# Kernel tuning notes

Hardware: AMD Instinct MI355X
Metric: run time of the kernel (lower is better)

The kernel has to match this reference:

```python
import jax, jax.numpy as jnp
import numpy as np

NUM_HEADS = 6
WIN = 16
NW = 16   # number of windows sharing one mask (b_ % NW == 0)


def setup_inputs() -> dict:
    key = jax.random.key(0)
    ks = jax.random.split(key, 6)
    b_, n, dim = 256, WIN * WIN, 192
    qkv = jax.random.normal(ks[0], (b_, n, 3 * dim), dtype=jnp.float32)
    rpi = jax.random.randint(ks[1], (n, n), 0, (2 * WIN - 1) * (2 * WIN - 1))
    # additive attention mask per window-group (Swin uses 0 / -100; randn is fine for math)
    mask = jax.random.normal(ks[2], (NW, n, n), dtype=jnp.float32)
    rpb_table = 0.02 * jax.random.normal(ks[3], ((2 * WIN - 1) * (2 * WIN - 1), NUM_HEADS), dtype=jnp.float32)
    proj_w = jax.random.normal(ks[4], (dim, dim), dtype=jnp.float32) * (1.0 / np.sqrt(dim))
    proj_b = jax.random.normal(ks[5], (dim,), dtype=jnp.float32) * 0.01
    return {"qkv": qkv, "rpi": rpi, "mask": mask, "rpb_table": rpb_table,
            "proj_w": proj_w, "proj_b": proj_b}


def reference(qkv, rpi, mask, rpb_table, proj_w, proj_b):
    b_, n, c3 = qkv.shape
    c = c3 // 3
    h = NUM_HEADS
    hd = c // h
    scale = float(hd) ** -0.5
    # (b_, n, 3, h, hd) -> (3, b_, h, n, hd)
    qkv = qkv.reshape(b_, n, 3, h, hd).transpose(2, 0, 3, 1, 4)
    q, k, v = qkv[0] * scale, qkv[1], qkv[2]
    attn = jnp.einsum('bhqd,bhkd->bhqk', q, k)  # [b_, h, n, n]
    # gathered relative position bias: [n, n, h] -> [h, n, n]
    bias = rpb_table[rpi].transpose(2, 0, 1)
    attn = attn + bias[None]
    # add per-window-group mask: [b_//nw, nw, h, n, n]
    nw = mask.shape[0]
    attn = attn.reshape(b_ // nw, nw, h, n, n) + mask[None, :, None]
    attn = attn.reshape(b_, h, n, n)
    attn = jax.nn.softmax(attn, axis=-1)
    x = jnp.einsum('bhqk,bhkd->bhqd', attn, v)  # [b_, h, n, hd]
    x = x.transpose(0, 2, 1, 3).reshape(b_, n, c)
    # nn.Linear: x @ W^T + b
    return x @ proj_w.T + proj_b
```

## Files before the change

### kernel.cpp

```cpp
#include <hip/hip_runtime.h>
#include <hip/hip_bf16.h>

typedef _Float16 f16;
typedef _Float16 f16x2 __attribute__((ext_vector_type(2)));
typedef _Float16 f16x4 __attribute__((ext_vector_type(4)));
typedef _Float16 f16x8 __attribute__((ext_vector_type(8)));
typedef __fp16 h16x2 __attribute__((ext_vector_type(2)));
typedef float f32x4 __attribute__((ext_vector_type(4)));

#define NHEADS 6
#define NTOK 256
#define NWINS 256
#define DIM 192
#define HD 32
#define C3 576
#define LOG2E 1.4426950408889634f
#define SCALE (0.17677669529663687f * LOG2E)

__device__ inline f16x2 pkrtz(float a, float b) {
  h16x2 r = __builtin_amdgcn_cvt_pkrtz(a, b);
  return __builtin_bit_cast(f16x2, r);
}

__global__ __launch_bounds__(256) void prep_cb_kernel(const int* __restrict__ rpi,
                                                      const float* __restrict__ mask,
                                                      const float* __restrict__ rpb,
                                                      f16* __restrict__ cb) {
  int idx = blockIdx.x * 256 + threadIdx.x;
  int k = idx & 255;
  int q = (idx >> 8) & 255;
  int t = idx >> 16;
  int h = t % 6;
  int mg = t / 6;
  float v = (rpb[rpi[(q << 8) | k] * 6 + h] + mask[(mg << 16) | (q << 8) | k]) * LOG2E;
  cb[idx] = (f16)v;
}

__global__ __launch_bounds__(256) void prep_w_kernel(const float* __restrict__ w,
                                                     f16* __restrict__ w16) {
  int i = blockIdx.x * 256 + threadIdx.x;
  if (i < DIM * DIM) w16[i] = (f16)w[i];
}

__device__ inline f16x8 q_to_f16(float4 a, float4 b) {
  f16x2 p0 = pkrtz(a.x * SCALE, a.y * SCALE);
  f16x2 p1 = pkrtz(a.z * SCALE, a.w * SCALE);
  f16x2 p2 = pkrtz(b.x * SCALE, b.y * SCALE);
  f16x2 p3 = pkrtz(b.z * SCALE, b.w * SCALE);
  f16x4 lo = __builtin_shufflevector(p0, p1, 0, 1, 2, 3);
  f16x4 hi = __builtin_shufflevector(p2, p3, 0, 1, 2, 3);
  return __builtin_shufflevector(lo, hi, 0, 1, 2, 3, 4, 5, 6, 7);
}

__global__ __launch_bounds__(256, 3) void attn_kernel(const float* __restrict__ qkv,
                                                      const f16* __restrict__ cb,
                                                      f16* __restrict__ x16) {
  const int idx = blockIdx.x;
  const int b = idx & 255;
  const int h = idx >> 8;
  const int tid = threadIdx.x;
  const int lane = tid & 63;
  const int wave = tid >> 6;
  const int g = lane >> 4;
  const int r16 = lane & 15;

  __shared__ f16 Klin[16 * 64 * 8];
  __shared__ f16 VT[32][264];

  const int qbase = wave * 64;
  const size_t cb_base = ((size_t)((b & 15) * 6 + h)) << 16;
  const f16* cbp = cb + cb_base + ((size_t)(qbase + r16) << 8) + g * 4;

  const int srow = tid >> 3;
  const int part = tid & 7;
  const float* kbase = qkv + (size_t)(b * NTOK + srow) * C3 + DIM + h * HD + part * 4;
  float4 ka[4], va[4], kb[4], vb[4];
#pragma unroll
  for (int rg = 0; rg < 4; ++rg) {
    const float* kp = kbase + (size_t)(rg * 32) * C3;
    ka[rg] = *(const float4*)kp;
    va[rg] = *(const float4*)(kp + DIM);
  }
#pragma unroll
  for (int rg = 0; rg < 4; ++rg) {
    const float* kp = kbase + (size_t)(rg * 32 + 128) * C3;
    kb[rg] = *(const float4*)kp;
    vb[rg] = *(const float4*)(kp + DIM);
  }

  f16x4 cv[16];
#pragma unroll
  for (int i = 0; i < 16; ++i) cv[i] = *((const f16x4*)(cbp + i * 16));

  const float* qp = qkv + (size_t)(b * NTOK + qbase + r16) * C3 + h * HD + g * 8;
  float4 qn0 = ((const float4*)qp)[0];
  float4 qn1 = ((const float4*)qp)[1];

  const int gg = part >> 1;
  const int half = part & 1;
  const int d0 = part * 4;
#pragma unroll
  for (int rg = 0; rg < 4; ++rg) {
    const int row = rg * 32 + srow;
    const int slot = ((row >> 4) * 64) + gg * 16 + ((row & 15) ^ (gg << 2));
    f16x2 k01 = pkrtz(ka[rg].x, ka[rg].y);
    f16x2 k23 = pkrtz(ka[rg].z, ka[rg].w);
    *((f16x4*)&Klin[slot * 8 + half * 4]) = __builtin_shufflevector(k01, k23, 0, 1, 2, 3);
    VT[d0 + 0][row ^ (((d0 + 0) & 7) << 2)] = (f16)va[rg].x;
    VT[d0 + 1][row ^ (((d0 + 1) & 7) << 2)] = (f16)va[rg].y;
    VT[d0 + 2][row ^ (((d0 + 2) & 7) << 2)] = (f16)va[rg].z;
    VT[d0 + 3][row ^ (((d0 + 3) & 7) << 2)] = (f16)va[rg].w;
  }
#pragma unroll
  for (int rg = 0; rg < 4; ++rg) {
    const int row = rg * 32 + srow + 128;
    const int slot = ((row >> 4) * 64) + gg * 16 + ((row & 15) ^ (gg << 2));
    f16x2 k01 = pkrtz(kb[rg].x, kb[rg].y);
    f16x2 k23 = pkrtz(kb[rg].z, kb[rg].w);
    *((f16x4*)&Klin[slot * 8 + half * 4]) = __builtin_shufflevector(k01, k23, 0, 1, 2, 3);
    VT[d0 + 0][row ^ (((d0 + 0) & 7) << 2)] = (f16)vb[rg].x;
    VT[d0 + 1][row ^ (((d0 + 1) & 7) << 2)] = (f16)vb[rg].y;
    VT[d0 + 2][row ^ (((d0 + 2) & 7) << 2)] = (f16)vb[rg].z;
    VT[d0 + 3][row ^ (((d0 + 3) & 7) << 2)] = (f16)vb[rg].w;
  }

  f16x8 qf = q_to_f16(qn0, qn1);

  __syncthreads();

  const int krd = (lane & 48) + ((lane & 15) ^ ((lane >> 2) & 12));

#pragma unroll
  for (int c = 0; c < 4; ++c) {
    f32x4 acc[16];
#pragma unroll
    for (int kt = 0; kt < 16; ++kt) {
      acc[kt][0] = 0.f; acc[kt][1] = 0.f; acc[kt][2] = 0.f; acc[kt][3] = 0.f;
    }
#pragma unroll
    for (int kt = 0; kt < 16; ++kt) {
      f16x8 af = *((const f16x8*)&Klin[(kt * 64 + krd) * 8]);
      acc[kt] = __builtin_amdgcn_mfma_f32_16x16x32_f16(af, qf, acc[kt], 0, 0, 0);
    }

    float m0 = -1e30f, m1 = -1e30f, m2 = -1e30f, m3 = -1e30f;
#pragma unroll
    for (int kt = 0; kt < 16; ++kt) {
      acc[kt][0] += (float)cv[kt][0];
      acc[kt][1] += (float)cv[kt][1];
      acc[kt][2] += (float)cv[kt][2];
      acc[kt][3] += (float)cv[kt][3];
      m0 = fmaxf(m0, acc[kt][0]);
      m1 = fmaxf(m1, acc[kt][1]);
      m2 = fmaxf(m2, acc[kt][2]);
      m3 = fmaxf(m3, acc[kt][3]);
    }

    if (c < 3) {
      const f16* cbn = cbp + (c + 1) * 4096;
#pragma unroll
      for (int i = 0; i < 16; ++i) cv[i] = *((const f16x4*)(cbn + i * 16));
      const float* qpn = qp + (size_t)((c + 1) * 16) * C3;
      qn0 = ((const float4*)qpn)[0];
      qn1 = ((const float4*)qpn)[1];
    }

    float m = fmaxf(fmaxf(m0, m1), fmaxf(m2, m3));
    m = fmaxf(m, __shfl_xor(m, 16));
    m = fmaxf(m, __shfl_xor(m, 32));

    float s0 = 0.f, s1 = 0.f, s2 = 0.f, s3 = 0.f;
#pragma unroll
    for (int kt = 0; kt < 16; ++kt) {
      float p0 = __builtin_amdgcn_exp2f(acc[kt][0] - m);
      float p1 = __builtin_amdgcn_exp2f(acc[kt][1] - m);
      float p2 = __builtin_amdgcn_exp2f(acc[kt][2] - m);
      float p3 = __builtin_amdgcn_exp2f(acc[kt][3] - m);
      acc[kt][0] = p0; acc[kt][1] = p1; acc[kt][2] = p2; acc[kt][3] = p3;
      s0 += p0; s1 += p1; s2 += p2; s3 += p3;
    }
    float s = (s0 + s1) + (s2 + s3);
    s += __shfl_xor(s, 16);
    s += __shfl_xor(s, 32);
    const float rinv = 1.0f / s;

    f32x4 xacc[2];
#pragma unroll
    for (int dt = 0; dt < 2; ++dt) {
      xacc[dt][0] = 0.f; xacc[dt][1] = 0.f; xacc[dt][2] = 0.f; xacc[dt][3] = 0.f;
    }
#pragma unroll
    for (int kt = 0; kt < 16; ++kt) {
      f16x2 p01 = pkrtz(acc[kt][0], acc[kt][1]);
      f16x2 p23 = pkrtz(acc[kt][2], acc[kt][3]);
      f16x4 pf = __builtin_shufflevector(p01, p23, 0, 1, 2, 3);
#pragma unroll
      for (int dt = 0; dt < 2; ++dt) {
        const int vrow = dt * 16 + r16;
        const int col = (kt * 16 + g * 4) ^ ((r16 & 7) << 2);
        f16x4 vf = *((const f16x4*)&VT[vrow][col]);
        xacc[dt] = __builtin_amdgcn_mfma_f32_16x16x16f16(vf, pf, xacc[dt], 0, 0, 0);
      }
    }

    f16* xp = x16 + (size_t)(b * NTOK + qbase + c * 16 + r16) * DIM + h * HD;
#pragma unroll
    for (int dt = 0; dt < 2; ++dt) {
      f16x2 o01 = pkrtz(xacc[dt][0] * rinv, xacc[dt][1] * rinv);
      f16x2 o23 = pkrtz(xacc[dt][2] * rinv, xacc[dt][3] * rinv);
      *((f16x4*)(xp + dt * 16 + g * 4)) = __builtin_shufflevector(o01, o23, 0, 1, 2, 3);
    }

    if (c < 3) qf = q_to_f16(qn0, qn1);
  }
}

__global__ __launch_bounds__(256) void proj_kernel(const f16* __restrict__ x16,
                                                   const f16* __restrict__ w16,
                                                   const float* __restrict__ pb,
                                                   float* __restrict__ out) {
  const int lane = threadIdx.x & 63;
  const int wave = threadIdx.x >> 6;
  const int g = lane >> 4;
  const int r16 = lane & 15;
  const int m0 = blockIdx.x * 64 + wave * 16;

  f32x4 acc[12];
#pragma unroll
  for (int jt = 0; jt < 12; ++jt) {
    acc[jt][0] = 0.f; acc[jt][1] = 0.f; acc[jt][2] = 0.f; acc[jt][3] = 0.f;
  }
#pragma unroll
  for (int cc = 0; cc < 6; ++cc) {
    f16x8 af = *((const f16x8*)(x16 + (size_t)(m0 + r16) * DIM + cc * 32 + g * 8));
#pragma unroll
    for (int jt = 0; jt < 12; ++jt) {
      f16x8 bf = *((const f16x8*)(w16 + (size_t)(jt * 16 + r16) * DIM + cc * 32 + g * 8));
      acc[jt] = __builtin_amdgcn_mfma_f32_16x16x32_f16(af, bf, acc[jt], 0, 0, 0);
    }
  }
#pragma unroll
  for (int jt = 0; jt < 12; ++jt) {
    int j = jt * 16 + r16;
    float bias = pb[j];
#pragma unroll
    for (int r = 0; r < 4; ++r) {
      out[(size_t)(m0 + g * 4 + r) * DIM + j] = acc[jt][r] + bias;
    }
  }
}

extern "C" void kernel_launch(void* const* d_in, const int* in_sizes, int n_in,
                              void* d_out, int out_size, void* d_ws, size_t ws_size,
                              hipStream_t stream) {
  const float* qkv  = (const float*)d_in[0];
  const int*   rpi  = (const int*)d_in[1];
  const float* mask = (const float*)d_in[2];
  const float* rpb  = (const float*)d_in[3];
  const float* pw   = (const float*)d_in[4];
  const float* pbv  = (const float*)d_in[5];
  float* out = (float*)d_out;

  char* ws = (char*)d_ws;
  f16* cb  = (f16*)ws;
  f16* x16 = (f16*)(ws + 12582912);
  f16* w16 = (f16*)(ws + 12582912 + 25165824);

  prep_cb_kernel<<<24576, 256, 0, stream>>>(rpi, mask, rpb, cb);
  prep_w_kernel<<<144, 256, 0, stream>>>(pw, w16);
  attn_kernel<<<1536, 256, 0, stream>>>(qkv, cb, x16);
  proj_kernel<<<1024, 256, 0, stream>>>(x16, w16, pbv, out);
}
```

Before: 122.3 us.

## Split key loop into two online-softmax halves to raise attention occupancy

Each 16-query chunk now handles its 256 keys as two halves of 128, using an online-softmax rescale (scA) to merge the two partial results. This halves the live accumulator and bias registers, allowing launch bounds to rise from 3 to 4 blocks per SIMD. The exchange is extra exp/rescale arithmetic, an additional cross-lane max reduction per chunk, and serialisation between the halves.

```diff
diff --git a/kernel.cpp b/kernel.cpp
--- a/kernel.cpp
+++ b/kernel.cpp
@@ -52,7 +52,7 @@
   return __builtin_shufflevector(lo, hi, 0, 1, 2, 3, 4, 5, 6, 7);
 }
 
-__global__ __launch_bounds__(256, 3) void attn_kernel(const float* __restrict__ qkv,
+__global__ __launch_bounds__(256, 4) void attn_kernel(const float* __restrict__ qkv,
                                                       const f16* __restrict__ cb,
                                                       f16* __restrict__ x16) {
   const int idx = blockIdx.x;
@@ -88,9 +88,9 @@
     vb[rg] = *(const float4*)(kp + DIM);
   }
 
-  f16x4 cv[16];
-#pragma unroll
-  for (int i = 0; i < 16; ++i) cv[i] = *((const f16x4*)(cbp + i * 16));
+  f16x4 cvA[8], cvB[8];
+#pragma unroll
+  for (int i = 0; i < 8; ++i) cvA[i] = *((const f16x4*)(cbp + i * 16));
 
   const float* qp = qkv + (size_t)(b * NTOK + qbase + r16) * C3 + h * HD + g * 8;
   float4 qn0 = ((const float4*)qp)[0];
@@ -132,46 +132,105 @@
 
 #pragma unroll
   for (int c = 0; c < 4; ++c) {
-    f32x4 acc[16];
-#pragma unroll
-    for (int kt = 0; kt < 16; ++kt) {
+    f32x4 acc[8];
+#pragma unroll
+    for (int kt = 0; kt < 8; ++kt) {
       acc[kt][0] = 0.f; acc[kt][1] = 0.f; acc[kt][2] = 0.f; acc[kt][3] = 0.f;
     }
 #pragma unroll
-    for (int kt = 0; kt < 16; ++kt) {
+    for (int kt = 0; kt < 8; ++kt) {
       f16x8 af = *((const f16x8*)&Klin[(kt * 64 + krd) * 8]);
       acc[kt] = __builtin_amdgcn_mfma_f32_16x16x32_f16(af, qf, acc[kt], 0, 0, 0);
     }
 
+    const f16* cbc = cbp + c * 4096;
+#pragma unroll
+    for (int i = 0; i < 8; ++i) cvB[i] = *((const f16x4*)(cbc + (8 + i) * 16));
+
     float m0 = -1e30f, m1 = -1e30f, m2 = -1e30f, m3 = -1e30f;
 #pragma unroll
-    for (int kt = 0; kt < 16; ++kt) {
-      acc[kt][0] += (float)cv[kt][0];
-      acc[kt][1] += (float)cv[kt][1];
-      acc[kt][2] += (float)cv[kt][2];
-      acc[kt][3] += (float)cv[kt][3];
+    for (int kt = 0; kt < 8; ++kt) {
+      acc[kt][0] += (float)cvA[kt][0];
+      acc[kt][1] += (float)cvA[kt][1];
+      acc[kt][2] += (float)cvA[kt][2];
+      acc[kt][3] += (float)cvA[kt][3];
       m0 = fmaxf(m0, acc[kt][0]);
       m1 = fmaxf(m1, acc[kt][1]);
       m2 = fmaxf(m2, acc[kt][2]);
       m3 = fmaxf(m3, acc[kt][3]);
     }
+    float mA = fmaxf(fmaxf(m0, m1), fmaxf(m2, m3));
+    mA = fmaxf(mA, __shfl_xor(mA, 16));
+    mA = fmaxf(mA, __shfl_xor(mA, 32));
+
+    float s0 = 0.f, s1 = 0.f, s2 = 0.f, s3 = 0.f;
+#pragma unroll
+    for (int kt = 0; kt < 8; ++kt) {
+      float p0 = __builtin_amdgcn_exp2f(acc[kt][0] - mA);
+      float p1 = __builtin_amdgcn_exp2f(acc[kt][1] - mA);
+      float p2 = __builtin_amdgcn_exp2f(acc[kt][2] - mA);
+      float p3 = __builtin_amdgcn_exp2f(acc[kt][3] - mA);
+      acc[kt][0] = p0; acc[kt][1] = p1; acc[kt][2] = p2; acc[kt][3] = p3;
+      s0 += p0; s1 += p1; s2 += p2; s3 += p3;
+    }
+    float sA = (s0 + s1) + (s2 + s3);
+
+    f32x4 xacc[2];
+    xacc[0][0] = 0.f; xacc[0][1] = 0.f; xacc[0][2] = 0.f; xacc[0][3] = 0.f;
+    xacc[1][0] = 0.f; xacc[1][1] = 0.f; xacc[1][2] = 0.f; xacc[1][3] = 0.f;
+#pragma unroll
+    for (int kt = 0; kt < 8; ++kt) {
+      f16x2 p01 = pkrtz(acc[kt][0], acc[kt][1]);
+      f16x2 p23 = pkrtz(acc[kt][2], acc[kt][3]);
+      f16x4 pf = __builtin_shufflevector(p01, p23, 0, 1, 2, 3);
+#pragma unroll
+      for (int dt = 0; dt < 2; ++dt) {
+        const int col = (kt * 16 + g * 4) ^ ((r16 & 7) << 2);
+        f16x4 vf = *((const f16x4*)&VT[dt * 16 + r16][col]);
+        xacc[dt] = __builtin_amdgcn_mfma_f32_16x16x16f16(vf, pf, xacc[dt], 0, 0, 0);
+      }
+    }
+
+#pragma unroll
+    for (int kt = 0; kt < 8; ++kt) {
+      acc[kt][0] = 0.f; acc[kt][1] = 0.f; acc[kt][2] = 0.f; acc[kt][3] = 0.f;
+    }
+#pragma unroll
+    for (int kt = 0; kt < 8; ++kt) {
+      f16x8 af = *((const f16x8*)&Klin[((kt + 8) * 64 + krd) * 8]);
+      acc[kt] = __builtin_amdgcn_mfma_f32_16x16x32_f16(af, qf, acc[kt], 0, 0, 0);
+    }
 
     if (c < 3) {
-      const f16* cbn = cbp + (c + 1) * 4096;
-#pragma unroll
-      for (int i = 0; i < 16; ++i) cv[i] = *((const f16x4*)(cbn + i * 16));
+#pragma unroll
+      for (int i = 0; i < 8; ++i) cvA[i] = *((const f16x4*)(cbc + 4096 + i * 16));
       const float* qpn = qp + (size_t)((c + 1) * 16) * C3;
       qn0 = ((const float4*)qpn)[0];
       qn1 = ((const float4*)qpn)[1];
     }
 
-    float m = fmaxf(fmaxf(m0, m1), fmaxf(m2, m3));
-    m = fmaxf(m, __shfl_xor(m, 16));
-    m = fmaxf(m, __shfl_xor(m, 32));
-
-    float s0 = 0.f, s1 = 0.f, s2 = 0.f, s3 = 0.f;
-#pragma unroll
-    for (int kt = 0; kt < 16; ++kt) {
+    m0 = -1e30f; m1 = -1e30f; m2 = -1e30f; m3 = -1e30f;
+#pragma unroll
+    for (int kt = 0; kt < 8; ++kt) {
+      acc[kt][0] += (float)cvB[kt][0];
+      acc[kt][1] += (float)cvB[kt][1];
+      acc[kt][2] += (float)cvB[kt][2];
+      acc[kt][3] += (float)cvB[kt][3];
+      m0 = fmaxf(m0, acc[kt][0]);
+      m1 = fmaxf(m1, acc[kt][1]);
+      m2 = fmaxf(m2, acc[kt][2]);
+      m3 = fmaxf(m3, acc[kt][3]);
+    }
+    float mB = fmaxf(fmaxf(m0, m1), fmaxf(m2, m3));
+    mB = fmaxf(mB, __shfl_xor(mB, 16));
+    mB = fmaxf(mB, __shfl_xor(mB, 32));
+
+    const float m = fmaxf(mA, mB);
+    const float scA = __builtin_amdgcn_exp2f(mA - m);
+
+    s0 = 0.f; s1 = 0.f; s2 = 0.f; s3 = 0.f;
+#pragma unroll
+    for (int kt = 0; kt < 8; ++kt) {
       float p0 = __builtin_amdgcn_exp2f(acc[kt][0] - m);
       float p1 = __builtin_amdgcn_exp2f(acc[kt][1] - m);
       float p2 = __builtin_amdgcn_exp2f(acc[kt][2] - m);
@@ -179,26 +238,22 @@
       acc[kt][0] = p0; acc[kt][1] = p1; acc[kt][2] = p2; acc[kt][3] = p3;
       s0 += p0; s1 += p1; s2 += p2; s3 += p3;
     }
-    float s = (s0 + s1) + (s2 + s3);
+    float s = sA * scA + (s0 + s1) + (s2 + s3);
     s += __shfl_xor(s, 16);
     s += __shfl_xor(s, 32);
     const float rinv = 1.0f / s;
 
-    f32x4 xacc[2];
-#pragma unroll
-    for (int dt = 0; dt < 2; ++dt) {
-      xacc[dt][0] = 0.f; xacc[dt][1] = 0.f; xacc[dt][2] = 0.f; xacc[dt][3] = 0.f;
-    }
-#pragma unroll
-    for (int kt = 0; kt < 16; ++kt) {
+    xacc[0][0] *= scA; xacc[0][1] *= scA; xacc[0][2] *= scA; xacc[0][3] *= scA;
+    xacc[1][0] *= scA; xacc[1][1] *= scA; xacc[1][2] *= scA; xacc[1][3] *= scA;
+#pragma unroll
+    for (int kt = 0; kt < 8; ++kt) {
       f16x2 p01 = pkrtz(acc[kt][0], acc[kt][1]);
       f16x2 p23 = pkrtz(acc[kt][2], acc[kt][3]);
       f16x4 pf = __builtin_shufflevector(p01, p23, 0, 1, 2, 3);
 #pragma unroll
       for (int dt = 0; dt < 2; ++dt) {
-        const int vrow = dt * 16 + r16;
-        const int col = (kt * 16 + g * 4) ^ ((r16 & 7) << 2);
-        f16x4 vf = *((const f16x4*)&VT[vrow][col]);
+        const int col = ((kt + 8) * 16 + g * 4) ^ ((r16 & 7) << 2);
+        f16x4 vf = *((const f16x4*)&VT[dt * 16 + r16][col]);
         xacc[dt] = __builtin_amdgcn_mfma_f32_16x16x16f16(vf, pf, xacc[dt], 0, 0, 0);
       }
     }
```

Measured after the change: 120.0 us. Within noise of the previous version (-2.0%).
